# Kernel optimization log

Hardware: AMD Instinct MI355X
Metric: run time of the kernel (lower is better)

The kernel has to match this reference:

```python
import jax, jax.numpy as jnp
import numpy as np

B, NQ, NV, DIM, HEADS, K = 2, 2048, 2048, 256, 8, 8
HD = DIM // HEADS
HID = 4 * DIM
SCALE = HD ** -0.5
EPS = 1e-5


def setup_inputs() -> dict:
    key = jax.random.key(0)
    ks = jax.random.split(key, 40)
    r = lambda i, s: jax.random.normal(ks[i], s, jnp.float32) * 0.02
    inp = {
        'q': jax.random.normal(ks[0], (B, NQ, DIM), jnp.float32),
        'v': jax.random.normal(ks[1], (B, NV, DIM), jnp.float32),
        'q_pos': jax.random.normal(ks[2], (B, NQ, 3), jnp.float32),
        'v_pos': jax.random.normal(ks[3], (B, NV, 3), jnp.float32),
        'self_knn_index': jax.random.randint(ks[4], (B, NQ, K), 0, NQ, jnp.int32),
        'cross_knn_index': jax.random.randint(ks[5], (B, NQ, K), 0, NV, jnp.int32),
        # LayerNorms (gamma=1, beta=0)
        'norm1_g': jnp.ones(DIM), 'norm1_b': jnp.zeros(DIM),
        'normq_g': jnp.ones(DIM), 'normq_b': jnp.zeros(DIM),
        'normv_g': jnp.ones(DIM), 'normv_b': jnp.zeros(DIM),
        'norm2_g': jnp.ones(DIM), 'norm2_b': jnp.zeros(DIM),
        # self-attention (qkv_bias=False), proj has bias
        'sa_qkv_w': r(6, (DIM, 3 * DIM)),
        'sa_proj_w': r(7, (DIM, DIM)), 'sa_proj_b': jnp.zeros(DIM),
        # cross-attention: q proj and kv proj (no bias), out proj with bias
        'ca_q_w': r(8, (DIM, DIM)),
        'ca_kv_w': r(9, (DIM, 2 * DIM)),
        'ca_proj_w': r(10, (DIM, DIM)), 'ca_proj_b': jnp.zeros(DIM),
        # MLP
        'fc1_w': r(11, (DIM, HID)), 'fc1_b': jnp.zeros(HID),
        'fc2_w': r(12, (HID, DIM)), 'fc2_b': jnp.zeros(DIM),
        # kNN maps
        'knn_w': r(13, (2 * DIM, DIM)), 'knn_b': jnp.zeros(DIM),
        'merge_w': r(14, (2 * DIM, DIM)), 'merge_b': jnp.zeros(DIM),
        'knnx_w': r(15, (2 * DIM, DIM)), 'knnx_b': jnp.zeros(DIM),
        'mergex_w': r(16, (2 * DIM, DIM)), 'mergex_b': jnp.zeros(DIM),
    }
    return inp


def _ln(x, g, b):
    m = x.mean(-1, keepdims=True)
    var = x.var(-1, keepdims=True)
    return (x - m) / jnp.sqrt(var + EPS) * g + b


def _heads(x):  # [B,N,DIM] -> [B,H,N,HD]
    Bx, N, _ = x.shape
    return x.reshape(Bx, N, HEADS, HD).transpose(0, 2, 1, 3)


def _attend(qh, kh, vh, proj_w, proj_b):
    a = jax.nn.softmax(jnp.einsum('bhqd,bhkd->bhqk', qh, kh) * SCALE, axis=-1)
    o = jnp.einsum('bhqk,bhkd->bhqd', a, vh)
    Bx, _, N, _ = o.shape
    o = o.transpose(0, 2, 1, 3).reshape(Bx, N, DIM)
    return o @ proj_w + proj_b


_gather = jax.vmap(lambda pts, idx: pts[idx])  # ([N,D],[Nq,K]) -> [Nq,K,D]


def _knn_feature(qn, vn, idx):  # gather -> diff/cat -> [B,Nq,K,2D]
    local = _gather(vn, idx)                      # [B,Nq,K,D]
    qe = qn[:, :, None, :]                        # [B,Nq,1,D]
    return jnp.concatenate([local - qe, jnp.broadcast_to(qe, local.shape)], -1)


def reference(q, v, q_pos, v_pos, self_knn_index, cross_knn_index,
              norm1_g, norm1_b, normq_g, normq_b, normv_g, normv_b,
              norm2_g, norm2_b, sa_qkv_w, sa_proj_w, sa_proj_b,
              ca_q_w, ca_kv_w, ca_proj_w, ca_proj_b,
              fc1_w, fc1_b, fc2_w, fc2_b,
              knn_w, knn_b, merge_w, merge_b,
              knnx_w, knnx_b, mergex_w, mergex_b):
    # ---- self-attention block with self-kNN branch ----
    nq = _ln(q, norm1_g, norm1_b)
    qkv = nq @ sa_qkv_w
    qh, kh, vh = (_heads(t) for t in jnp.split(qkv, 3, axis=-1))
    sa_out = _attend(qh, kh, vh, sa_proj_w, sa_proj_b)
    f = _knn_feature(nq, nq, self_knn_index)
    knn_out = jax.nn.leaky_relu(f @ knn_w + knn_b, 0.2).max(axis=-2)
    q1 = jnp.concatenate([sa_out, knn_out], -1) @ merge_w + merge_b
    q = q + q1
    # ---- cross-attention block with cross-kNN branch ----
    nq2 = _ln(q, normq_g, normq_b)
    nv = _ln(v, normv_g, normv_b)
    qh = _heads(nq2 @ ca_q_w)
    kh, vh = (_heads(t) for t in jnp.split(nv @ ca_kv_w, 2, axis=-1))
    ca_out = _attend(qh, kh, vh, ca_proj_w, ca_proj_b)
    f = _knn_feature(nq2, nv, cross_knn_index)
    knnx_out = jax.nn.leaky_relu(f @ knnx_w + knnx_b, 0.2).max(axis=-2)
    q2 = jnp.concatenate([ca_out, knnx_out], -1) @ mergex_w + mergex_b
    q = q + q2
    # ---- MLP block ----
    h = _ln(q, norm2_g, norm2_b)
    h = jax.nn.gelu(h @ fc1_w + fc1_b, approximate=False)
    q = q + (h @ fc2_w + fc2_b)
    return q
```

## Files before the change

kernel.cpp:

```cpp
#include <hip/hip_runtime.h>
#include <math.h>

#define NQC   2048
#define NKVC  2048
#define DIMC  256
#define SCALEF 0.17677669529663687f

typedef short bfrag __attribute__((ext_vector_type(8)));
typedef float ffrag __attribute__((ext_vector_type(4)));
typedef unsigned short us8 __attribute__((ext_vector_type(8)));

__device__ __forceinline__ float gelu_exact(float x) {
    return 0.5f * x * (1.0f + erff(x * 0.70710678118654752f));
}
__device__ __forceinline__ unsigned short f2bf(float f) {
    union { float f; unsigned u; } v; v.f = f;
    unsigned r = v.u + 0x7FFFu + ((v.u >> 16) & 1u);
    return (unsigned short)(r >> 16);
}
__device__ __forceinline__ float bf2f(unsigned short u) {
    union { unsigned u; float f; } v; v.u = ((unsigned)u) << 16;
    return v.f;
}

__global__ __launch_bounds__(256) void prep_w(
    const float* __restrict__ qkv, const float* __restrict__ knn,
    const float* __restrict__ proj, const float* __restrict__ merge,
    const float* __restrict__ caq, const float* __restrict__ knnx,
    const float* __restrict__ cakv, const float* __restrict__ projx,
    const float* __restrict__ mergex, const float* __restrict__ fc1,
    const float* __restrict__ fc2, unsigned short* __restrict__ dst)
{
    int e = (blockIdx.x * 256 + threadIdx.x) * 4;
    float v[4];
    float scale = 1.0f;
    if (e < 327680) {
        int n = e >> 8, k = e & 255;
        if (n < 768) {
            const float* s = qkv + (size_t)k * 768 + n;
            #pragma unroll
            for (int i = 0; i < 4; ++i) v[i] = s[(size_t)i * 768];
            if (n < 256) scale = SCALEF;
        } else if (n < 1024) {
            const float* s = knn + (size_t)k * 256 + (n - 768);
            #pragma unroll
            for (int i = 0; i < 4; ++i) v[i] = s[(size_t)i * 256];
        } else {
            const float* s = knn + (size_t)k * 256 + (n - 1024);
            #pragma unroll
            for (int i = 0; i < 4; ++i) v[i] = s[65536 + (size_t)i * 256] - s[(size_t)i * 256];
        }
    } else if (e < 393216) {
        int l = e - 327680, n = l >> 8, k = l & 255;
        const float* s = proj + (size_t)k * 256 + n;
        #pragma unroll
        for (int i = 0; i < 4; ++i) v[i] = s[(size_t)i * 256];
    } else if (e < 524288) {
        int l = e - 393216, n = l >> 9, k = l & 511;
        const float* s = merge + (size_t)k * 256 + n;
        #pragma unroll
        for (int i = 0; i < 4; ++i) v[i] = s[(size_t)i * 256];
    } else if (e < 655360) {
        int l = e - 524288, n = l >> 8, k = l & 255;
        if (n < 256) {
            const float* s = caq + (size_t)k * 256 + n;
            #pragma unroll
            for (int i = 0; i < 4; ++i) v[i] = s[(size_t)i * 256];
            scale = SCALEF;
        } else {
            const float* s = knnx + (size_t)k * 256 + (n - 256);
            #pragma unroll
            for (int i = 0; i < 4; ++i) v[i] = s[65536 + (size_t)i * 256] - s[(size_t)i * 256];
        }
    } else if (e < 851968) {
        int l = e - 655360, n = l >> 8, k = l & 255;
        if (n < 512) {
            const float* s = cakv + (size_t)k * 512 + n;
            #pragma unroll
            for (int i = 0; i < 4; ++i) v[i] = s[(size_t)i * 512];
        } else {
            const float* s = knnx + (size_t)k * 256 + (n - 512);
            #pragma unroll
            for (int i = 0; i < 4; ++i) v[i] = s[(size_t)i * 256];
        }
    } else if (e < 917504) {
        int l = e - 851968, n = l >> 8, k = l & 255;
        const float* s = projx + (size_t)k * 256 + n;
        #pragma unroll
        for (int i = 0; i < 4; ++i) v[i] = s[(size_t)i * 256];
    } else if (e < 1048576) {
        int l = e - 917504, n = l >> 9, k = l & 511;
        const float* s = mergex + (size_t)k * 256 + n;
        #pragma unroll
        for (int i = 0; i < 4; ++i) v[i] = s[(size_t)i * 256];
    } else if (e < 1310720) {
        int l = e - 1048576, n = l >> 8, k = l & 255;
        const float* s = fc1 + (size_t)k * 1024 + n;
        #pragma unroll
        for (int i = 0; i < 4; ++i) v[i] = s[(size_t)i * 1024];
    } else {
        int l = e - 1310720, n = l >> 10, k = l & 1023;
        const float* s = fc2 + (size_t)k * 256 + n;
        #pragma unroll
        for (int i = 0; i < 4; ++i) v[i] = s[(size_t)i * 256];
    }
    ushort4 o;
    o.x = f2bf(v[0] * scale); o.y = f2bf(v[1] * scale);
    o.z = f2bf(v[2] * scale); o.w = f2bf(v[3] * scale);
    *(ushort4*)(dst + e) = o;
}

__global__ __launch_bounds__(256) void ln_b(
    const float* __restrict__ x, const float* __restrict__ g,
    const float* __restrict__ b, unsigned short* __restrict__ y)
{
    int wid = threadIdx.x >> 6, lane = threadIdx.x & 63;
    int row = blockIdx.x * 4 + wid;
    const float* xr = x + (size_t)row * DIMC + lane * 4;
    float4 vv = *(const float4*)xr;
    float s  = vv.x + vv.y + vv.z + vv.w;
    float sq = vv.x*vv.x + vv.y*vv.y + vv.z*vv.z + vv.w*vv.w;
    #pragma unroll
    for (int off = 32; off >= 1; off >>= 1) {
        s  += __shfl_xor(s, off);
        sq += __shfl_xor(sq, off);
    }
    float mean = s * (1.0f/DIMC);
    float var  = sq * (1.0f/DIMC) - mean*mean;
    float inv  = rsqrtf(var + 1e-5f);
    float4 gg = *(const float4*)(g + lane*4);
    float4 bb = *(const float4*)(b + lane*4);
    ushort4 o;
    o.x = f2bf((vv.x - mean) * inv * gg.x + bb.x);
    o.y = f2bf((vv.y - mean) * inv * gg.y + bb.y);
    o.z = f2bf((vv.z - mean) * inv * gg.z + bb.z);
    o.w = f2bf((vv.w - mean) * inv * gg.w + bb.w);
    *(ushort4*)(y + (size_t)row * DIMC + lane * 4) = o;
}

template<int ACT, int RESID, int OUTBF>
__global__ __launch_bounds__(256) void gemm64(
    const unsigned short* __restrict__ A, int lda,
    const unsigned short* __restrict__ Wt,
    const float* __restrict__ bias,
    const float* __restrict__ resid, int ldr,
    void* __restrict__ Cp, int ldc, int Kc)
{
    __shared__ unsigned short Alds[64][72];
    __shared__ unsigned short Wlds[64][72];
    const int tid = threadIdx.x;
    const int wid = tid >> 6, lane = tid & 63;
    const int lm = lane & 15, quad = lane >> 4;
    const int wr = wid >> 1, wc = wid & 1;
    const int row0 = blockIdx.y * 64, col0 = blockIdx.x * 64;
    const int ar = tid >> 2, ac = (tid & 3) * 16;
    const unsigned short* Ag = A  + (size_t)(row0 + ar) * lda + ac;
    const unsigned short* Wg = Wt + (size_t)(col0 + ar) * Kc  + ac;

    us8 a0 = *(const us8*)Ag;
    us8 a1 = *(const us8*)(Ag + 8);
    us8 w0 = *(const us8*)Wg;
    us8 w1 = *(const us8*)(Wg + 8);

    ffrag acc[2][2];
    #pragma unroll
    for (int mi = 0; mi < 2; ++mi)
        #pragma unroll
        for (int ni = 0; ni < 2; ++ni)
            acc[mi][ni] = (ffrag){0.f, 0.f, 0.f, 0.f};

    for (int k0 = 0;;) {
        __syncthreads();
        *(us8*)&Alds[ar][ac]   = a0;
        *(us8*)&Alds[ar][ac+8] = a1;
        *(us8*)&Wlds[ar][ac]   = w0;
        *(us8*)&Wlds[ar][ac+8] = w1;
        __syncthreads();
        k0 += 64;
        if (k0 < Kc) {
            a0 = *(const us8*)(Ag + k0);
            a1 = *(const us8*)(Ag + k0 + 8);
            w0 = *(const us8*)(Wg + k0);
            w1 = *(const us8*)(Wg + k0 + 8);
        }
        #pragma unroll
        for (int kc = 0; kc < 2; ++kc) {
            bfrag af[2], bw[2];
            #pragma unroll
            for (int mi = 0; mi < 2; ++mi)
                af[mi] = *(const bfrag*)&Alds[wr*32 + mi*16 + lm][kc*32 + quad*8];
            #pragma unroll
            for (int ni = 0; ni < 2; ++ni)
                bw[ni] = *(const bfrag*)&Wlds[wc*32 + ni*16 + lm][kc*32 + quad*8];
            #pragma unroll
            for (int mi = 0; mi < 2; ++mi)
                #pragma unroll
                for (int ni = 0; ni < 2; ++ni)
                    acc[mi][ni] = __builtin_amdgcn_mfma_f32_16x16x32_bf16(
                        af[mi], bw[ni], acc[mi][ni], 0, 0, 0);
        }
        if (k0 >= Kc) break;
    }
    #pragma unroll
    for (int mi = 0; mi < 2; ++mi) {
        #pragma unroll
        for (int ni = 0; ni < 2; ++ni) {
            int gr = row0 + wr*32 + mi*16 + quad*4;
            int gc = col0 + wc*32 + ni*16 + lm;
            float bv = bias ? bias[gc] : 0.f;
            #pragma unroll
            for (int r = 0; r < 4; ++r) {
                float o = acc[mi][ni][r] + bv;
                if (ACT == 1) o = gelu_exact(o);
                if (RESID) o += resid[(size_t)(gr + r) * ldr + gc];
                if (OUTBF) ((unsigned short*)Cp)[(size_t)(gr + r) * ldc + gc] = f2bf(o);
                else       ((float*)Cp)[(size_t)(gr + r) * ldc + gc] = o;
            }
        }
    }
}

__global__ __launch_bounds__(256) void attn_bf16(
    const unsigned short* __restrict__ Qp, int ldq,
    const unsigned short* __restrict__ Kp, int ldk,
    const unsigned short* __restrict__ Vp, int ldv,
    unsigned short* __restrict__ Op, int ldo)
{
    __shared__ unsigned short Klds[64][40];
    __shared__ unsigned short Vt[32][72];
    __shared__ unsigned short Plds[4][16][72];
    int bb = blockIdx.z, h = blockIdx.y;
    int hoff = h * 32;
    int tid = threadIdx.x, wid = tid >> 6, lane = tid & 63;
    int lm = lane & 15, quad = lane >> 4;
    size_t qbase  = (size_t)bb * NQC;
    size_t kvbase = (size_t)bb * NKVC;
    int q0 = blockIdx.x * 64 + wid * 16;

    bfrag aq = *(const bfrag*)(Qp + (qbase + q0 + lm) * (size_t)ldq + hoff + quad * 8);

    float l_r[4] = {0.f, 0.f, 0.f, 0.f};
    ffrag oacc[2];
    oacc[0] = (ffrag){0.f, 0.f, 0.f, 0.f};
    oacc[1] = (ffrag){0.f, 0.f, 0.f, 0.f};

    const int kkey = tid >> 2, kd0 = (tid & 3) * 8;
    const int vkey = tid & 63, vd0 = (tid >> 6) * 8;
    const unsigned short* kg0 = Kp + (kvbase + kkey) * (size_t)ldk + hoff + kd0;
    const unsigned short* vg0 = Vp + (kvbase + vkey) * (size_t)ldv + hoff + vd0;

    for (int kt = 0; kt < NKVC / 64; ++kt) {
        us8 kv = *(const us8*)(kg0 + (size_t)kt * 64 * ldk);
        us8 vv = *(const us8*)(vg0 + (size_t)kt * 64 * ldv);
        __syncthreads();
        *(us8*)&Klds[kkey][kd0] = kv;
        #pragma unroll
        for (int i = 0; i < 8; ++i) Vt[vd0 + i][vkey] = vv[i];
        __syncthreads();

        ffrag sacc[4];
        #pragma unroll
        for (int t = 0; t < 4; ++t) {
            bfrag bk = *(const bfrag*)&Klds[t*16 + lm][quad * 8];
            sacc[t] = __builtin_amdgcn_mfma_f32_16x16x32_bf16(
                aq, bk, (ffrag){0.f,0.f,0.f,0.f}, 0, 0, 0);
        }

        #pragma unroll
        for (int r = 0; r < 4; ++r) {
            float p0 = __expf(sacc[0][r]), p1 = __expf(sacc[1][r]);
            float p2 = __expf(sacc[2][r]), p3 = __expf(sacc[3][r]);
            l_r[r] += (p0 + p1) + (p2 + p3);
            int row = quad * 4 + r;
            Plds[wid][row][lm +  0] = f2bf(p0);
            Plds[wid][row][lm + 16] = f2bf(p1);
            Plds[wid][row][lm + 32] = f2bf(p2);
            Plds[wid][row][lm + 48] = f2bf(p3);
        }
        asm volatile("s_waitcnt lgkmcnt(0)" ::: "memory");

        #pragma unroll
        for (int kc = 0; kc < 2; ++kc) {
            bfrag ap = *(const bfrag*)&Plds[wid][lm][kc*32 + quad*8];
            #pragma unroll
            for (int nt = 0; nt < 2; ++nt) {
                bfrag bv = *(const bfrag*)&Vt[nt*16 + lm][kc*32 + quad*8];
                oacc[nt] = __builtin_amdgcn_mfma_f32_16x16x32_bf16(
                    ap, bv, oacc[nt], 0, 0, 0);
            }
        }
    }
    #pragma unroll
    for (int r = 0; r < 4; ++r) {
        float l = l_r[r];
        l += __shfl_xor(l, 1);
        l += __shfl_xor(l, 2);
        l += __shfl_xor(l, 4);
        l += __shfl_xor(l, 8);
        l_r[r] = 1.0f / l;
    }
    #pragma unroll
    for (int nt = 0; nt < 2; ++nt)
        #pragma unroll
        for (int r = 0; r < 4; ++r) {
            float ov = oacc[nt][r] * l_r[r];
            Op[(qbase + q0 + quad*4 + r) * (size_t)ldo + hoff + nt*16 + lm] = f2bf(ov);
        }
}

__global__ __launch_bounds__(256) void gathermax_b(
    const unsigned short* __restrict__ P, int ldp,
    const unsigned short* __restrict__ Base, int ldb,
    const float* __restrict__ bias, const int* __restrict__ idx,
    unsigned short* __restrict__ out, int ldo)
{
    int wid = threadIdx.x >> 6, lane = threadIdx.x & 63;
    int q = blockIdx.x * 4 + wid;
    int b = q >> 11;
    int c = lane * 4;
    ushort4 bu = *(const ushort4*)(Base + (size_t)q * ldb + c);
    float4 bi = *(const float4*)(bias + c);
    float bsx = bf2f(bu.x) + bi.x, bsy = bf2f(bu.y) + bi.y;
    float bsz = bf2f(bu.z) + bi.z, bsw = bf2f(bu.w) + bi.w;
    float4 acc = make_float4(-3e38f, -3e38f, -3e38f, -3e38f);
    const int* ip = idx + (size_t)q * 8;
    #pragma unroll
    for (int k = 0; k < 8; ++k) {
        int j = ip[k];
        ushort4 pu = *(const ushort4*)(P + ((size_t)(b * NKVC + j)) * ldp + c);
        float t;
        t = bsx + bf2f(pu.x); t = t > 0.f ? t : 0.2f * t; acc.x = fmaxf(acc.x, t);
        t = bsy + bf2f(pu.y); t = t > 0.f ? t : 0.2f * t; acc.y = fmaxf(acc.y, t);
        t = bsz + bf2f(pu.z); t = t > 0.f ? t : 0.2f * t; acc.z = fmaxf(acc.z, t);
        t = bsw + bf2f(pu.w); t = t > 0.f ? t : 0.2f * t; acc.w = fmaxf(acc.w, t);
    }
    ushort4 o;
    o.x = f2bf(acc.x); o.y = f2bf(acc.y); o.z = f2bf(acc.z); o.w = f2bf(acc.w);
    *(ushort4*)(out + (size_t)q * ldo + c) = o;
}

extern "C" void kernel_launch(void* const* d_in, const int* in_sizes, int n_in,
                              void* d_out, int out_size, void* d_ws, size_t ws_size,
                              hipStream_t stream) {
    const float* q_in   = (const float*)d_in[0];
    const float* v_in   = (const float*)d_in[1];
    const int*   idx_s  = (const int*)d_in[4];
    const int*   idx_x  = (const int*)d_in[5];
    const float* n1g = (const float*)d_in[6],  *n1b = (const float*)d_in[7];
    const float* nqg = (const float*)d_in[8],  *nqb = (const float*)d_in[9];
    const float* nvg = (const float*)d_in[10], *nvb = (const float*)d_in[11];
    const float* n2g = (const float*)d_in[12], *n2b = (const float*)d_in[13];
    const float* sa_qkv_w  = (const float*)d_in[14];
    const float* sa_proj_w = (const float*)d_in[15];
    const float* sa_proj_b = (const float*)d_in[16];
    const float* ca_q_w    = (const float*)d_in[17];
    const float* ca_kv_w   = (const float*)d_in[18];
    const float* ca_proj_w = (const float*)d_in[19];
    const float* ca_proj_b = (const float*)d_in[20];
    const float* fc1_w = (const float*)d_in[21], *fc1_b = (const float*)d_in[22];
    const float* fc2_w = (const float*)d_in[23], *fc2_b = (const float*)d_in[24];
    const float* knn_w   = (const float*)d_in[25], *knn_b   = (const float*)d_in[26];
    const float* merge_w = (const float*)d_in[27], *merge_b = (const float*)d_in[28];
    const float* knnx_w  = (const float*)d_in[29], *knnx_b  = (const float*)d_in[30];
    const float* mergex_w = (const float*)d_in[31], *mergex_b = (const float*)d_in[32];
    float* out = (float*)d_out;

    unsigned short* A1      = (unsigned short*)d_ws;
    unsigned short* A2      = A1;
    unsigned short* A3      = A1 + (size_t)4096 * 512;
    unsigned short* Hb      = A1;
    unsigned short* attnraw = A1 + (size_t)4096 * 1280;
    unsigned short* CC      = attnraw + (size_t)4096 * 256;
    unsigned short* XB      = CC + (size_t)4096 * 512;
    unsigned short* NVB     = XB + (size_t)4096 * 256;
    unsigned short* WT      = NVB + (size_t)4096 * 256;
    unsigned short* WT1     = WT;
    unsigned short* WTproj  = WT + 327680;
    unsigned short* WTmerge = WT + 393216;
    unsigned short* WT2     = WT + 524288;
    unsigned short* WT3     = WT + 655360;
    unsigned short* WTprojx = WT + 851968;
    unsigned short* WTmergex= WT + 917504;
    unsigned short* WTfc1   = WT + 1048576;
    unsigned short* WTfc2   = WT + 1310720;

    dim3 blk(256);
    dim3 gAttn(NQC / 64, 8, 2);

    prep_w<<<dim3(1536), blk, 0, stream>>>(sa_qkv_w, knn_w, sa_proj_w, merge_w,
        ca_q_w, knnx_w, ca_kv_w, ca_proj_w, mergex_w, fc1_w, fc2_w, WT);

    ln_b<<<dim3(1024), blk, 0, stream>>>(q_in, n1g, n1b, XB);
    gemm64<0,0,1><<<dim3(20,64), blk, 0, stream>>>(XB, 256, WT1,
        nullptr, nullptr, 0, A1, 1280, 256);
    attn_bf16<<<gAttn, blk, 0, stream>>>(A1, 1280, A1+256, 1280, A1+512, 1280,
        attnraw, 256);
    gathermax_b<<<dim3(1024), blk, 0, stream>>>(A1+768, 1280, A1+1024, 1280,
        knn_b, idx_s, CC+256, 512);
    gemm64<0,0,1><<<dim3(4,64), blk, 0, stream>>>(attnraw, 256, WTproj,
        sa_proj_b, nullptr, 0, CC, 512, 256);
    gemm64<0,1,0><<<dim3(4,64), blk, 0, stream>>>(CC, 512, WTmerge,
        merge_b, q_in, 256, out, 256, 512);

    ln_b<<<dim3(1024), blk, 0, stream>>>(out, nqg, nqb, XB);
    ln_b<<<dim3(1024), blk, 0, stream>>>(v_in, nvg, nvb, NVB);
    gemm64<0,0,1><<<dim3(8,64), blk, 0, stream>>>(XB, 256, WT2,
        nullptr, nullptr, 0, A2, 512, 256);
    gemm64<0,0,1><<<dim3(12,64), blk, 0, stream>>>(NVB, 256, WT3,
        nullptr, nullptr, 0, A3, 768, 256);
    attn_bf16<<<gAttn, blk, 0, stream>>>(A2, 512, A3, 768, A3+256, 768,
        attnraw, 256);
    gathermax_b<<<dim3(1024), blk, 0, stream>>>(A3+512, 768, A2+256, 512,
        knnx_b, idx_x, CC+256, 512);
    gemm64<0,0,1><<<dim3(4,64), blk, 0, stream>>>(attnraw, 256, WTprojx,
        ca_proj_b, nullptr, 0, CC, 512, 256);
    gemm64<0,1,0><<<dim3(4,64), blk, 0, stream>>>(CC, 512, WTmergex,
        mergex_b, out, 256, out, 256, 512);

    ln_b<<<dim3(1024), blk, 0, stream>>>(out, n2g, n2b, XB);
    gemm64<1,0,1><<<dim3(16,64), blk, 0, stream>>>(XB, 256, WTfc1,
        fc1_b, nullptr, 0, Hb, 1024, 256);
    gemm64<0,1,0><<<dim3(4,64), blk, 0, stream>>>(Hb, 1024, WTfc2,
        fc2_b, out, 256, out, 256, 1024);
}
```

Before: 289.0 us.

## Split attention over KV chunks and fuse LayerNorm into GEMM prologue

```diff
diff --git a/kernel.cpp b/kernel.cpp
--- a/kernel.cpp
+++ b/kernel.cpp
@@ -108,34 +108,6 @@
     o.x = f2bf(v[0] * scale); o.y = f2bf(v[1] * scale);
     o.z = f2bf(v[2] * scale); o.w = f2bf(v[3] * scale);
     *(ushort4*)(dst + e) = o;
-}
-
-__global__ __launch_bounds__(256) void ln_b(
-    const float* __restrict__ x, const float* __restrict__ g,
-    const float* __restrict__ b, unsigned short* __restrict__ y)
-{
-    int wid = threadIdx.x >> 6, lane = threadIdx.x & 63;
-    int row = blockIdx.x * 4 + wid;
-    const float* xr = x + (size_t)row * DIMC + lane * 4;
-    float4 vv = *(const float4*)xr;
-    float s  = vv.x + vv.y + vv.z + vv.w;
-    float sq = vv.x*vv.x + vv.y*vv.y + vv.z*vv.z + vv.w*vv.w;
-    #pragma unroll
-    for (int off = 32; off >= 1; off >>= 1) {
-        s  += __shfl_xor(s, off);
-        sq += __shfl_xor(sq, off);
-    }
-    float mean = s * (1.0f/DIMC);
-    float var  = sq * (1.0f/DIMC) - mean*mean;
-    float inv  = rsqrtf(var + 1e-5f);
-    float4 gg = *(const float4*)(g + lane*4);
-    float4 bb = *(const float4*)(b + lane*4);
-    ushort4 o;
-    o.x = f2bf((vv.x - mean) * inv * gg.x + bb.x);
-    o.y = f2bf((vv.y - mean) * inv * gg.y + bb.y);
-    o.z = f2bf((vv.z - mean) * inv * gg.z + bb.z);
-    o.w = f2bf((vv.w - mean) * inv * gg.w + bb.w);
-    *(ushort4*)(y + (size_t)row * DIMC + lane * 4) = o;
 }
 
 template<int ACT, int RESID, int OUTBF>
@@ -220,16 +192,122 @@
     }
 }
 
-__global__ __launch_bounds__(256) void attn_bf16(
+template<int ACT>
+__global__ __launch_bounds__(256) void gemm64_ln(
+    const float* __restrict__ X,
+    const float* __restrict__ g, const float* __restrict__ b,
+    const unsigned short* __restrict__ Wt,
+    const float* __restrict__ bias,
+    unsigned short* __restrict__ C, int ldc)
+{
+    __shared__ unsigned short Alds[64][264];
+    __shared__ unsigned short Wlds[64][72];
+    const int tid = threadIdx.x;
+    const int wid = tid >> 6, lane = tid & 63;
+    const int lm = lane & 15, quad = lane >> 4;
+    const int wr = wid >> 1, wc = wid & 1;
+    const int row0 = blockIdx.y * 64, col0 = blockIdx.x * 64;
+
+    const int rr = tid >> 2, c0 = (tid & 3) * 64;
+    const float* xp = X + (size_t)(row0 + rr) * 256 + c0;
+    float s = 0.f, sq = 0.f;
+    #pragma unroll
+    for (int i = 0; i < 16; ++i) {
+        float4 v = *(const float4*)(xp + i * 4);
+        s  += (v.x + v.y) + (v.z + v.w);
+        sq += (v.x*v.x + v.y*v.y) + (v.z*v.z + v.w*v.w);
+    }
+    s  += __shfl_xor(s, 1);  sq += __shfl_xor(sq, 1);
+    s  += __shfl_xor(s, 2);  sq += __shfl_xor(sq, 2);
+    float mean = s * (1.0f/256.0f);
+    float inv  = rsqrtf(sq * (1.0f/256.0f) - mean*mean + 1e-5f);
+    #pragma unroll
+    for (int j = 0; j < 8; ++j) {
+        float4 v0 = *(const float4*)(xp + j*8);
+        float4 v1 = *(const float4*)(xp + j*8 + 4);
+        float4 g0 = *(const float4*)(g + c0 + j*8);
+        float4 g1 = *(const float4*)(g + c0 + j*8 + 4);
+        float4 b0 = *(const float4*)(b + c0 + j*8);
+        float4 b1 = *(const float4*)(b + c0 + j*8 + 4);
+        us8 w;
+        w[0] = f2bf((v0.x - mean) * inv * g0.x + b0.x);
+        w[1] = f2bf((v0.y - mean) * inv * g0.y + b0.y);
+        w[2] = f2bf((v0.z - mean) * inv * g0.z + b0.z);
+        w[3] = f2bf((v0.w - mean) * inv * g0.w + b0.w);
+        w[4] = f2bf((v1.x - mean) * inv * g1.x + b1.x);
+        w[5] = f2bf((v1.y - mean) * inv * g1.y + b1.y);
+        w[6] = f2bf((v1.z - mean) * inv * g1.z + b1.z);
+        w[7] = f2bf((v1.w - mean) * inv * g1.w + b1.w);
+        *(us8*)&Alds[rr][c0 + j*8] = w;
+    }
+
+    const int ar = tid >> 2, ac = (tid & 3) * 16;
+    const unsigned short* Wg = Wt + (size_t)(col0 + ar) * 256 + ac;
+    us8 w0 = *(const us8*)Wg;
+    us8 w1 = *(const us8*)(Wg + 8);
+
+    ffrag acc[2][2];
+    #pragma unroll
+    for (int mi = 0; mi < 2; ++mi)
+        #pragma unroll
+        for (int ni = 0; ni < 2; ++ni)
+            acc[mi][ni] = (ffrag){0.f, 0.f, 0.f, 0.f};
+
+    #pragma unroll
+    for (int k0 = 0; k0 < 256; k0 += 64) {
+        __syncthreads();
+        *(us8*)&Wlds[ar][ac]   = w0;
+        *(us8*)&Wlds[ar][ac+8] = w1;
+        __syncthreads();
+        if (k0 + 64 < 256) {
+            w0 = *(const us8*)(Wg + k0 + 64);
+            w1 = *(const us8*)(Wg + k0 + 72);
+        }
+        #pragma unroll
+        for (int kc = 0; kc < 2; ++kc) {
+            bfrag af[2], bw[2];
+            #pragma unroll
+            for (int mi = 0; mi < 2; ++mi)
+                af[mi] = *(const bfrag*)&Alds[wr*32 + mi*16 + lm][k0 + kc*32 + quad*8];
+            #pragma unroll
+            for (int ni = 0; ni < 2; ++ni)
+                bw[ni] = *(const bfrag*)&Wlds[wc*32 + ni*16 + lm][kc*32 + quad*8];
+            #pragma unroll
+            for (int mi = 0; mi < 2; ++mi)
+                #pragma unroll
+                for (int ni = 0; ni < 2; ++ni)
+                    acc[mi][ni] = __builtin_amdgcn_mfma_f32_16x16x32_bf16(
+                        af[mi], bw[ni], acc[mi][ni], 0, 0, 0);
+        }
+    }
+    #pragma unroll
+    for (int mi = 0; mi < 2; ++mi) {
+        #pragma unroll
+        for (int ni = 0; ni < 2; ++ni) {
+            int gr = row0 + wr*32 + mi*16 + quad*4;
+            int gc = col0 + wc*32 + ni*16 + lm;
+            float bv = bias ? bias[gc] : 0.f;
+            #pragma unroll
+            for (int r = 0; r < 4; ++r) {
+                float o = acc[mi][ni][r] + bv;
+                if (ACT == 1) o = gelu_exact(o);
+                C[(size_t)(gr + r) * ldc + gc] = f2bf(o);
+            }
+        }
+    }
+}
+
+__global__ __launch_bounds__(256) void attn_part(
     const unsigned short* __restrict__ Qp, int ldq,
     const unsigned short* __restrict__ Kp, int ldk,
     const unsigned short* __restrict__ Vp, int ldv,
-    unsigned short* __restrict__ Op, int ldo)
+    float* __restrict__ Op, float* __restrict__ Lp)
 {
     __shared__ unsigned short Klds[64][40];
     __shared__ unsigned short Vt[32][72];
     __shared__ unsigned short Plds[4][16][72];
-    int bb = blockIdx.z, h = blockIdx.y;
+    int zc = blockIdx.z, bb = zc >> 1, ck = zc & 1;
+    int h = blockIdx.y;
     int hoff = h * 32;
     int tid = threadIdx.x, wid = tid >> 6, lane = tid & 63;
     int lm = lane & 15, quad = lane >> 4;
@@ -249,7 +327,7 @@
     const unsigned short* kg0 = Kp + (kvbase + kkey) * (size_t)ldk + hoff + kd0;
     const unsigned short* vg0 = Vp + (kvbase + vkey) * (size_t)ldv + hoff + vd0;
 
-    for (int kt = 0; kt < NKVC / 64; ++kt) {
+    for (int kt = ck * 16; kt < ck * 16 + 16; ++kt) {
         us8 kv = *(const us8*)(kg0 + (size_t)kt * 64 * ldk);
         us8 vv = *(const us8*)(vg0 + (size_t)kt * 64 * ldv);
         __syncthreads();
@@ -291,21 +369,39 @@
         }
     }
     #pragma unroll
+    for (int nt = 0; nt < 2; ++nt)
+        #pragma unroll
+        for (int r = 0; r < 4; ++r)
+            Op[((size_t)ck * 4096 + qbase + q0 + quad*4 + r) * 256 + hoff + nt*16 + lm]
+                = oacc[nt][r];
+    #pragma unroll
     for (int r = 0; r < 4; ++r) {
         float l = l_r[r];
         l += __shfl_xor(l, 1);
         l += __shfl_xor(l, 2);
         l += __shfl_xor(l, 4);
         l += __shfl_xor(l, 8);
-        l_r[r] = 1.0f / l;
-    }
-    #pragma unroll
-    for (int nt = 0; nt < 2; ++nt)
-        #pragma unroll
-        for (int r = 0; r < 4; ++r) {
-            float ov = oacc[nt][r] * l_r[r];
-            Op[(qbase + q0 + quad*4 + r) * (size_t)ldo + hoff + nt*16 + lm] = f2bf(ov);
-        }
+        if (lm == 0)
+            Lp[((size_t)ck * 4096 + qbase + q0 + quad*4 + r) * 8 + h] = l;
+    }
+}
+
+__global__ __launch_bounds__(256) void attn_comb(
+    const float* __restrict__ Op, const float* __restrict__ Lp,
+    unsigned short* __restrict__ dst)
+{
+    int wid = threadIdx.x >> 6, lane = threadIdx.x & 63;
+    int row = blockIdx.x * 4 + wid;
+    int c = lane * 4, h = c >> 5;
+    float4 o0 = *(const float4*)(Op + (size_t)row * 256 + c);
+    float4 o1 = *(const float4*)(Op + (size_t)(4096 + row) * 256 + c);
+    float inv = 1.0f / (Lp[(size_t)row * 8 + h] + Lp[(size_t)(4096 + row) * 8 + h]);
+    ushort4 o;
+    o.x = f2bf((o0.x + o1.x) * inv);
+    o.y = f2bf((o0.y + o1.y) * inv);
+    o.z = f2bf((o0.z + o1.z) * inv);
+    o.w = f2bf((o0.w + o1.w) * inv);
+    *(ushort4*)(dst + (size_t)row * 256 + c) = o;
 }
 
 __global__ __launch_bounds__(256) void gathermax_b(
@@ -371,9 +467,7 @@
     unsigned short* Hb      = A1;
     unsigned short* attnraw = A1 + (size_t)4096 * 1280;
     unsigned short* CC      = attnraw + (size_t)4096 * 256;
-    unsigned short* XB      = CC + (size_t)4096 * 512;
-    unsigned short* NVB     = XB + (size_t)4096 * 256;
-    unsigned short* WT      = NVB + (size_t)4096 * 256;
+    unsigned short* WT      = CC + (size_t)4096 * 512;
     unsigned short* WT1     = WT;
     unsigned short* WTproj  = WT + 327680;
     unsigned short* WTmerge = WT + 393216;
@@ -383,18 +477,20 @@
     unsigned short* WTmergex= WT + 917504;
     unsigned short* WTfc1   = WT + 1048576;
     unsigned short* WTfc2   = WT + 1310720;
+    float* Opart = (float*)(WT + 1572864);
+    float* Lpart = Opart + (size_t)2 * 4096 * 256;
 
     dim3 blk(256);
-    dim3 gAttn(NQC / 64, 8, 2);
+    dim3 gAttn(NQC / 64, 8, 4);
 
     prep_w<<<dim3(1536), blk, 0, stream>>>(sa_qkv_w, knn_w, sa_proj_w, merge_w,
         ca_q_w, knnx_w, ca_kv_w, ca_proj_w, mergex_w, fc1_w, fc2_w, WT);
 
-    ln_b<<<dim3(1024), blk, 0, stream>>>(q_in, n1g, n1b, XB);
-    gemm64<0,0,1><<<dim3(20,64), blk, 0, stream>>>(XB, 256, WT1,
-        nullptr, nullptr, 0, A1, 1280, 256);
-    attn_bf16<<<gAttn, blk, 0, stream>>>(A1, 1280, A1+256, 1280, A1+512, 1280,
-        attnraw, 256);
+    gemm64_ln<0><<<dim3(20,64), blk, 0, stream>>>(q_in, n1g, n1b, WT1,
+        nullptr, A1, 1280);
+    attn_part<<<gAttn, blk, 0, stream>>>(A1, 1280, A1+256, 1280, A1+512, 1280,
+        Opart, Lpart);
+    attn_comb<<<dim3(1024), blk, 0, stream>>>(Opart, Lpart, attnraw);
     gathermax_b<<<dim3(1024), blk, 0, stream>>>(A1+768, 1280, A1+1024, 1280,
         knn_b, idx_s, CC+256, 512);
     gemm64<0,0,1><<<dim3(4,64), blk, 0, stream>>>(attnraw, 256, WTproj,
@@ -402,14 +498,13 @@
     gemm64<0,1,0><<<dim3(4,64), blk, 0, stream>>>(CC, 512, WTmerge,
         merge_b, q_in, 256, out, 256, 512);
 
-    ln_b<<<dim3(1024), blk, 0, stream>>>(out, nqg, nqb, XB);
-    ln_b<<<dim3(1024), blk, 0, stream>>>(v_in, nvg, nvb, NVB);
-    gemm64<0,0,1><<<dim3(8,64), blk, 0, stream>>>(XB, 256, WT2,
-        nullptr, nullptr, 0, A2, 512, 256);
-    gemm64<0,0,1><<<dim3(12,64), blk, 0, stream>>>(NVB, 256, WT3,
-        nullptr, nullptr, 0, A3, 768, 256);
-    attn_bf16<<<gAttn, blk, 0, stream>>>(A2, 512, A3, 768, A3+256, 768,
-        attnraw, 256);
+    gemm64_ln<0><<<dim3(8,64), blk, 0, stream>>>(out, nqg, nqb, WT2,
+        nullptr, A2, 512);
+    gemm64_ln<0><<<dim3(12,64), blk, 0, stream>>>(v_in, nvg, nvb, WT3,
+        nullptr, A3, 768);
+    attn_part<<<gAttn, blk, 0, stream>>>(A2, 512, A3, 768, A3+256, 768,
+        Opart, Lpart);
+    attn_comb<<<dim3(1024), blk, 0, stream>>>(Opart, Lpart, attnraw);
     gathermax_b<<<dim3(1024), blk, 0, stream>>>(A3+512, 768, A2+256, 512,
         knnx_b, idx_x, CC+256, 512);
     gemm64<0,0,1><<<dim3(4,64), blk, 0, stream>>>(attnraw, 256, WTprojx,
@@ -417,9 +512,8 @@
     gemm64<0,1,0><<<dim3(4,64), blk, 0, stream>>>(CC, 512, WTmergex,
         mergex_b, out, 256, out, 256, 512);
 
-    ln_b<<<dim3(1024), blk, 0, stream>>>(out, n2g, n2b, XB);
-    gemm64<1,0,1><<<dim3(16,64), blk, 0, stream>>>(XB, 256, WTfc1,
-        fc1_b, nullptr, 0, Hb, 1024, 256);
+    gemm64_ln<1><<<dim3(16,64), blk, 0, stream>>>(out, n2g, n2b, WTfc1,
+        fc1_b, Hb, 1024);
     gemm64<0,1,0><<<dim3(4,64), blk, 0, stream>>>(Hb, 1024, WTfc2,
         fc2_b, out, 256, out, 256, 1024);
 }
```

Measured after the change: 408.8 us. +41.5%, slower.

## Split attention over two key chunks and combine partial results

Applied to the files above, without the earlier changes.

```diff
diff --git a/kernel.cpp b/kernel.cpp
--- a/kernel.cpp
+++ b/kernel.cpp
@@ -220,16 +220,17 @@
     }
 }
 
-__global__ __launch_bounds__(256) void attn_bf16(
+__global__ __launch_bounds__(256) void attn_part(
     const unsigned short* __restrict__ Qp, int ldq,
     const unsigned short* __restrict__ Kp, int ldk,
     const unsigned short* __restrict__ Vp, int ldv,
-    unsigned short* __restrict__ Op, int ldo)
+    unsigned short* __restrict__ Op, float* __restrict__ Lp)
 {
     __shared__ unsigned short Klds[64][40];
     __shared__ unsigned short Vt[32][72];
     __shared__ unsigned short Plds[4][16][72];
-    int bb = blockIdx.z, h = blockIdx.y;
+    int zc = blockIdx.z, bb = zc >> 1, ck = zc & 1;
+    int h = blockIdx.y;
     int hoff = h * 32;
     int tid = threadIdx.x, wid = tid >> 6, lane = tid & 63;
     int lm = lane & 15, quad = lane >> 4;
@@ -249,7 +250,7 @@
     const unsigned short* kg0 = Kp + (kvbase + kkey) * (size_t)ldk + hoff + kd0;
     const unsigned short* vg0 = Vp + (kvbase + vkey) * (size_t)ldv + hoff + vd0;
 
-    for (int kt = 0; kt < NKVC / 64; ++kt) {
+    for (int kt = ck * 16; kt < ck * 16 + 16; ++kt) {
         us8 kv = *(const us8*)(kg0 + (size_t)kt * 64 * ldk);
         us8 vv = *(const us8*)(vg0 + (size_t)kt * 64 * ldv);
         __syncthreads();
@@ -291,21 +292,39 @@
         }
     }
     #pragma unroll
+    for (int nt = 0; nt < 2; ++nt)
+        #pragma unroll
+        for (int r = 0; r < 4; ++r)
+            Op[((size_t)ck * 4096 + qbase + q0 + quad*4 + r) * 256 + hoff + nt*16 + lm]
+                = f2bf(oacc[nt][r]);
+    #pragma unroll
     for (int r = 0; r < 4; ++r) {
         float l = l_r[r];
         l += __shfl_xor(l, 1);
         l += __shfl_xor(l, 2);
         l += __shfl_xor(l, 4);
         l += __shfl_xor(l, 8);
-        l_r[r] = 1.0f / l;
-    }
-    #pragma unroll
-    for (int nt = 0; nt < 2; ++nt)
-        #pragma unroll
-        for (int r = 0; r < 4; ++r) {
-            float ov = oacc[nt][r] * l_r[r];
-            Op[(qbase + q0 + quad*4 + r) * (size_t)ldo + hoff + nt*16 + lm] = f2bf(ov);
-        }
+        if (lm == 0)
+            Lp[((size_t)ck * 4096 + qbase + q0 + quad*4 + r) * 8 + h] = l;
+    }
+}
+
+__global__ __launch_bounds__(256) void attn_comb(
+    const unsigned short* __restrict__ Op, const float* __restrict__ Lp,
+    unsigned short* __restrict__ dst)
+{
+    int wid = threadIdx.x >> 6, lane = threadIdx.x & 63;
+    int row = blockIdx.x * 4 + wid;
+    int c = lane * 4, h = c >> 5;
+    ushort4 o0 = *(const ushort4*)(Op + (size_t)row * 256 + c);
+    ushort4 o1 = *(const ushort4*)(Op + (size_t)(4096 + row) * 256 + c);
+    float inv = 1.0f / (Lp[(size_t)row * 8 + h] + Lp[(size_t)(4096 + row) * 8 + h]);
+    ushort4 o;
+    o.x = f2bf((bf2f(o0.x) + bf2f(o1.x)) * inv);
+    o.y = f2bf((bf2f(o0.y) + bf2f(o1.y)) * inv);
+    o.z = f2bf((bf2f(o0.z) + bf2f(o1.z)) * inv);
+    o.w = f2bf((bf2f(o0.w) + bf2f(o1.w)) * inv);
+    *(ushort4*)(dst + (size_t)row * 256 + c) = o;
 }
 
 __global__ __launch_bounds__(256) void gathermax_b(
@@ -383,9 +402,11 @@
     unsigned short* WTmergex= WT + 917504;
     unsigned short* WTfc1   = WT + 1048576;
     unsigned short* WTfc2   = WT + 1310720;
+    unsigned short* Opart   = WT + 1572864;
+    float* Lpart = (float*)(Opart + (size_t)2 * 4096 * 256);
 
     dim3 blk(256);
-    dim3 gAttn(NQC / 64, 8, 2);
+    dim3 gAttn(NQC / 64, 8, 4);
 
     prep_w<<<dim3(1536), blk, 0, stream>>>(sa_qkv_w, knn_w, sa_proj_w, merge_w,
         ca_q_w, knnx_w, ca_kv_w, ca_proj_w, mergex_w, fc1_w, fc2_w, WT);
@@ -393,8 +414,9 @@
     ln_b<<<dim3(1024), blk, 0, stream>>>(q_in, n1g, n1b, XB);
     gemm64<0,0,1><<<dim3(20,64), blk, 0, stream>>>(XB, 256, WT1,
         nullptr, nullptr, 0, A1, 1280, 256);
-    attn_bf16<<<gAttn, blk, 0, stream>>>(A1, 1280, A1+256, 1280, A1+512, 1280,
-        attnraw, 256);
+    attn_part<<<gAttn, blk, 0, stream>>>(A1, 1280, A1+256, 1280, A1+512, 1280,
+        Opart, Lpart);
+    attn_comb<<<dim3(1024), blk, 0, stream>>>(Opart, Lpart, attnraw);
     gathermax_b<<<dim3(1024), blk, 0, stream>>>(A1+768, 1280, A1+1024, 1280,
         knn_b, idx_s, CC+256, 512);
     gemm64<0,0,1><<<dim3(4,64), blk, 0, stream>>>(attnraw, 256, WTproj,
@@ -408,8 +430,9 @@
         nullptr, nullptr, 0, A2, 512, 256);
     gemm64<0,0,1><<<dim3(12,64), blk, 0, stream>>>(NVB, 256, WT3,
         nullptr, nullptr, 0, A3, 768, 256);
-    attn_bf16<<<gAttn, blk, 0, stream>>>(A2, 512, A3, 768, A3+256, 768,
-        attnraw, 256);
+    attn_part<<<gAttn, blk, 0, stream>>>(A2, 512, A3, 768, A3+256, 768,
+        Opart, Lpart);
+    attn_comb<<<dim3(1024), blk, 0, stream>>>(Opart, Lpart, attnraw);
     gathermax_b<<<dim3(1024), blk, 0, stream>>>(A3+512, 768, A2+256, 512,
         knnx_b, idx_x, CC+256, 512);
     gemm64<0,0,1><<<dim3(4,64), blk, 0, stream>>>(attnraw, 256, WTprojx,
```

Result: faster. 277.8 us (-3.9%).
